# Optimization experiments

Measured on AMD Instinct MI355X. Metric: run time of the kernel, lower is better.

## Reference

```python
import math
import jax, jax.numpy as jnp
import numpy as np

E = 64   # embed_size (also per-head dim)
H = 8    # heads
B = 4
T = 2048


def setup_inputs() -> dict:
    key = jax.random.key(0)
    ks = jax.random.split(key, 8)
    s_in = 1.0 / math.sqrt(E)
    s_out = 1.0 / math.sqrt(H * E)
    return {
        "values": jax.random.normal(ks[0], (B, T, E), dtype=jnp.float32),
        "keys": jax.random.normal(ks[1], (B, T, E), dtype=jnp.float32),
        "queries": jax.random.normal(ks[2], (B, T, E), dtype=jnp.float32),
        # Linear(E, E*H, bias=False) weights, stored as [in, out] for x @ W
        "Wv": jax.random.uniform(ks[3], (E, E * H), jnp.float32, -s_in, s_in),
        "Wk": jax.random.uniform(ks[4], (E, E * H), jnp.float32, -s_in, s_in),
        "Wq": jax.random.uniform(ks[5], (E, E * H), jnp.float32, -s_in, s_in),
        # unifyheads: Linear(H*E, E)
        "Wu": jax.random.uniform(ks[6], (H * E, E), jnp.float32, -s_out, s_out),
        "bu": jax.random.uniform(ks[7], (E,), jnp.float32, -s_out, s_out),
    }


def reference(values, keys, queries, Wv, Wk, Wq, Wu, bu):
    b, t, e = keys.shape
    h = H
    v = (values @ Wv).reshape(b, t, h, e)   # bthe
    k = (keys @ Wk).reshape(b, t, h, e)
    q = (queries @ Wq).reshape(b, t, h, e)
    dot = jnp.einsum('bthe,bihe->bhti', q, k) / math.sqrt(e)  # [b,h,t,i]
    # NOTE: source applies softmax over dim=2 (the query axis t), faithfully kept
    attention = jax.nn.softmax(dot, axis=2)
    out = jnp.einsum('bhtd,bdhe->bthe', attention, v).reshape(b, t, h * e)
    return out @ Wu + bu
```

## Files before the change

### kernel.cpp

```cpp
#include <hip/hip_runtime.h>
#include <hip/hip_bf16.h>


typedef __attribute__((ext_vector_type(8))) __bf16 bf16x8;
typedef __attribute__((ext_vector_type(8))) unsigned short ushort8;
typedef __attribute__((ext_vector_type(4))) float f32x4;
typedef unsigned int uint32;

constexpr int B_ = 4;
constexpr int T_ = 2048;
constexpr int H_ = 8;
constexpr int E_ = 64;
constexpr int BH_ = B_ * H_;
constexpr float SCALE_ = 0.125f;

__device__ inline uint32 f2bf1(float f) {
  uint32 u = __builtin_bit_cast(uint32, f);
  return (u + 0x7fffu + ((u >> 16) & 1u)) >> 16;
}
__device__ inline uint32 pk2(float a, float b) {
  return f2bf1(a) | (f2bf1(b) << 16);
}
__device__ inline bf16x8 ld8(const unsigned short* p) {
  return __builtin_bit_cast(bf16x8, *(const ushort8*)p);
}
#define MFMA16(a, b, c) __builtin_amdgcn_mfma_f32_16x16x32_bf16(a, b, c, 0, 0, 0)

__global__ __launch_bounds__(512) void proj_bf16_kernel(
    const float* __restrict__ X, const float* __restrict__ W,
    unsigned short* __restrict__ Y, float scale) {
  constexpr int RT = 8;
  __shared__ float xs[RT][E_];
  const int row0 = blockIdx.x * RT;
  const int tid = threadIdx.x;
  {
    const int r = tid >> 6, c = tid & 63;
    xs[r][c] = X[(row0 + r) * E_ + c];
  }
  __syncthreads();
  const int j = tid;
  const int h = j >> 6, e = j & 63;
  float acc[RT];
#pragma unroll
  for (int r = 0; r < RT; ++r) acc[r] = 0.f;
  for (int c = 0; c < E_; ++c) {
    const float w = W[c * (H_ * E_) + j];
#pragma unroll
    for (int r = 0; r < RT; ++r) acc[r] += xs[r][c] * w;
  }
#pragma unroll
  for (int r = 0; r < RT; ++r) {
    const int row = row0 + r;
    const int b = row >> 11, t = row & (T_ - 1);
    Y[(((size_t)(b * H_ + h) * T_ + t) << 6) + e] =
        (unsigned short)f2bf1(acc[r] * scale);
  }
}

__global__ __launch_bounds__(512) void proj_f32_kernel(
    const float* __restrict__ X, const float* __restrict__ W,
    float* __restrict__ Y) {
  constexpr int RT = 8;
  __shared__ float xs[RT][E_];
  const int row0 = blockIdx.x * RT;
  const int tid = threadIdx.x;
  {
    const int r = tid >> 6, c = tid & 63;
    xs[r][c] = X[(row0 + r) * E_ + c];
  }
  __syncthreads();
  const int j = tid;
  const int h = j >> 6, e = j & 63;
  float acc[RT];
#pragma unroll
  for (int r = 0; r < RT; ++r) acc[r] = 0.f;
  for (int c = 0; c < E_; ++c) {
    const float w = W[c * (H_ * E_) + j];
#pragma unroll
    for (int r = 0; r < RT; ++r) acc[r] += xs[r][c] * w;
  }
#pragma unroll
  for (int r = 0; r < RT; ++r) {
    const int row = row0 + r;
    const int b = row >> 11, t = row & (T_ - 1);
    Y[(((size_t)(b * H_ + h) * T_ + t) << 6) + e] = acc[r];
  }
}

__global__ __launch_bounds__(256) void stats_kernel(
    const unsigned short* __restrict__ K16, const unsigned short* __restrict__ Q16,
    float* __restrict__ s_inv) {
  const int bh = blockIdx.y;
  const int tid = threadIdx.x;
  const int w = tid >> 6, lane = tid & 63;
  const int lm = lane & 15, lq = lane >> 4;
  const int d0 = blockIdx.x * 256 + w * 64;
  const unsigned short* Kp = K16 + (size_t)bh * T_ * E_;
  const unsigned short* Qp = Q16 + (size_t)bh * T_ * E_;

  bf16x8 kf[4][2];
#pragma unroll
  for (int dt = 0; dt < 4; ++dt) {
    kf[dt][0] = ld8(&Kp[(size_t)(d0 + dt * 16 + lm) * E_ + lq * 8]);
    kf[dt][1] = ld8(&Kp[(size_t)(d0 + dt * 16 + lm) * E_ + 32 + lq * 8]);
  }
  f32x4 sacc[4];
#pragma unroll
  for (int dt = 0; dt < 4; ++dt) sacc[dt] = (f32x4){0.f, 0.f, 0.f, 0.f};
  const f32x4 zero = {0.f, 0.f, 0.f, 0.f};

  for (int t0 = 0; t0 < T_; t0 += 16) {
    bf16x8 ql = ld8(&Qp[(size_t)(t0 + lm) * E_ + lq * 8]);
    bf16x8 qh = ld8(&Qp[(size_t)(t0 + lm) * E_ + 32 + lq * 8]);
#pragma unroll
    for (int dt = 0; dt < 4; ++dt) {
      f32x4 c = MFMA16(kf[dt][0], ql, zero);
      c = MFMA16(kf[dt][1], qh, c);
#pragma unroll
      for (int r = 0; r < 4; ++r) sacc[dt][r] += __expf(c[r]);
    }
  }
#pragma unroll
  for (int m = 1; m < 16; m <<= 1) {
#pragma unroll
    for (int dt = 0; dt < 4; ++dt)
#pragma unroll
      for (int r = 0; r < 4; ++r)
        sacc[dt][r] += __shfl_xor(sacc[dt][r], m);
  }
  if (lm == 0) {
#pragma unroll
    for (int dt = 0; dt < 4; ++dt)
#pragma unroll
      for (int r = 0; r < 4; ++r)
        s_inv[(size_t)bh * T_ + d0 + dt * 16 + lq * 4 + r] = 1.0f / sacc[dt][r];
  }
}

__global__ __launch_bounds__(256) void scale_kernel(
    const float* __restrict__ Vf, const float* __restrict__ s_inv,
    unsigned short* __restrict__ Vt16) {
  __shared__ float ts[64][68];
  const int bh = blockIdx.y;
  const int d0 = blockIdx.x * 64;
  const float* Vp = Vf + (size_t)bh * T_ * E_;
  const int tid = threadIdx.x;
  for (int idx = tid; idx < 64 * 16; idx += 256) {
    const int r = idx >> 4, c4 = idx & 15;
    const float4 v = *(const float4*)&Vp[(size_t)(d0 + r) * E_ + c4 * 4];
    const float is = s_inv[(size_t)bh * T_ + d0 + r];
    ts[r][c4 * 4 + 0] = v.x * is;
    ts[r][c4 * 4 + 1] = v.y * is;
    ts[r][c4 * 4 + 2] = v.z * is;
    ts[r][c4 * 4 + 3] = v.w * is;
  }
  __syncthreads();
  for (int idx = tid; idx < 64 * 16; idx += 256) {
    const int e = idx >> 4, d4 = idx & 15;
    uint2 o;
    o.x = pk2(ts[d4 * 4 + 0][e], ts[d4 * 4 + 1][e]);
    o.y = pk2(ts[d4 * 4 + 2][e], ts[d4 * 4 + 3][e]);
    *(uint2*)&Vt16[((size_t)bh * E_ + e) * T_ + d0 + d4 * 4] = o;
  }
}

__global__ __launch_bounds__(256) void apply_kernel(
    const unsigned short* __restrict__ K16, const unsigned short* __restrict__ Q16,
    const unsigned short* __restrict__ Vt16, float* __restrict__ o_ws) {
  __shared__ unsigned short es[4][32][40];
  const int bh = blockIdx.y;
  const int b = bh >> 3, h = bh & 7;
  const int tid = threadIdx.x;
  const int w = tid >> 6, lane = tid & 63;
  const int lm = lane & 15, lq = lane >> 4;
  const int t0 = blockIdx.x * 128 + w * 32;
  const unsigned short* Kp = K16 + (size_t)bh * T_ * E_;
  const unsigned short* Qp = Q16 + (size_t)bh * T_ * E_;
  const unsigned short* Vp = Vt16 + (size_t)bh * E_ * T_;

  bf16x8 qf[2][2];
#pragma unroll
  for (int tt = 0; tt < 2; ++tt) {
    qf[tt][0] = ld8(&Qp[(size_t)(t0 + tt * 16 + lm) * E_ + lq * 8]);
    qf[tt][1] = ld8(&Qp[(size_t)(t0 + tt * 16 + lm) * E_ + 32 + lq * 8]);
  }
  f32x4 acc[2][4];
#pragma unroll
  for (int tt = 0; tt < 2; ++tt)
#pragma unroll
    for (int ec = 0; ec < 4; ++ec) acc[tt][ec] = (f32x4){0.f, 0.f, 0.f, 0.f};
  const f32x4 zero = {0.f, 0.f, 0.f, 0.f};

  for (int d0 = 0; d0 < T_; d0 += 32) {
    const bf16x8 k0l = ld8(&Kp[(size_t)(d0 + lm) * E_ + lq * 8]);
    const bf16x8 k0h = ld8(&Kp[(size_t)(d0 + lm) * E_ + 32 + lq * 8]);
    const bf16x8 k1l = ld8(&Kp[(size_t)(d0 + 16 + lm) * E_ + lq * 8]);
    const bf16x8 k1h = ld8(&Kp[(size_t)(d0 + 16 + lm) * E_ + 32 + lq * 8]);
    bf16x8 vf[4];
#pragma unroll
    for (int ec = 0; ec < 4; ++ec)
      vf[ec] = ld8(&Vp[(size_t)(ec * 16 + lm) * T_ + d0 + lq * 8]);

#pragma unroll
    for (int tt = 0; tt < 2; ++tt) {
      f32x4 c0 = MFMA16(k0l, qf[tt][0], zero);
      c0 = MFMA16(k0h, qf[tt][1], c0);
      f32x4 c1 = MFMA16(k1l, qf[tt][0], zero);
      c1 = MFMA16(k1h, qf[tt][1], c1);
      float e0[4], e1[4];
#pragma unroll
      for (int r = 0; r < 4; ++r) { e0[r] = __expf(c0[r]); e1[r] = __expf(c1[r]); }
      *(uint2*)&es[w][tt * 16 + lm][lq * 4] =
          make_uint2(pk2(e0[0], e0[1]), pk2(e0[2], e0[3]));
      *(uint2*)&es[w][tt * 16 + lm][16 + lq * 4] =
          make_uint2(pk2(e1[0], e1[1]), pk2(e1[2], e1[3]));
    }
    asm volatile("s_waitcnt lgkmcnt(0)" ::: "memory");
#pragma unroll
    for (int tt = 0; tt < 2; ++tt) {
      const bf16x8 ae = ld8(&es[w][tt * 16 + lm][lq * 8]);
#pragma unroll
      for (int ec = 0; ec < 4; ++ec)
        acc[tt][ec] = MFMA16(ae, vf[ec], acc[tt][ec]);
    }
  }

#pragma unroll
  for (int tt = 0; tt < 2; ++tt) {
    const int t = t0 + tt * 16 + lq * 4;
#pragma unroll
    for (int ec = 0; ec < 4; ++ec) {
      const int e = ec * 16 + lm;
      float* op = &o_ws[((size_t)(b * T_ + t) * H_ + h) * E_ + e];
#pragma unroll
      for (int r = 0; r < 4; ++r) op[(size_t)r * H_ * E_] = acc[tt][ec][r];
    }
  }
}

__global__ __launch_bounds__(256) void unify_kernel(
    const float* __restrict__ o_ws, const float* __restrict__ Wu,
    const float* __restrict__ bu, float* __restrict__ out) {
  constexpr int RT = 16;
  __shared__ float xs[RT][H_ * E_];
  const int row0 = blockIdx.x * RT;
  const int tid = threadIdx.x;
  for (int idx = tid; idx < RT * 128; idx += 256) {
    const int r = idx >> 7, c4 = idx & 127;
    *(float4*)&xs[r][c4 * 4] = *(const float4*)&o_ws[(size_t)(row0 + r) * 512 + c4 * 4];
  }
  __syncthreads();
  const int j = tid & 63;
  const int rg = tid >> 6;
  float acc[4] = {0.f, 0.f, 0.f, 0.f};
  for (int c = 0; c < 512; ++c) {
    const float w = Wu[c * 64 + j];
#pragma unroll
    for (int r = 0; r < 4; ++r) acc[r] += xs[rg * 4 + r][c] * w;
  }
  const float bias = bu[j];
#pragma unroll
  for (int r = 0; r < 4; ++r)
    out[(size_t)(row0 + rg * 4 + r) * 64 + j] = acc[r] + bias;
}

extern "C" void kernel_launch(void* const* d_in, const int* in_sizes, int n_in,
                              void* d_out, int out_size, void* d_ws, size_t ws_size,
                              hipStream_t stream) {
  const float* values  = (const float*)d_in[0];
  const float* keys    = (const float*)d_in[1];
  const float* queries = (const float*)d_in[2];
  const float* Wv      = (const float*)d_in[3];
  const float* Wk      = (const float*)d_in[4];
  const float* Wq      = (const float*)d_in[5];
  const float* Wu      = (const float*)d_in[6];
  const float* bu      = (const float*)d_in[7];
  float* out = (float*)d_out;

  const size_t NQ = (size_t)BH_ * T_ * E_;
  unsigned short* q_bf = (unsigned short*)d_ws;
  unsigned short* k_bf = q_bf + NQ;
  unsigned short* vt_bf = k_bf + NQ;
  float* v_f  = (float*)(vt_bf + NQ);
  float* o_ws = v_f + NQ;
  float* s_inv = o_ws + NQ;

  proj_bf16_kernel<<<B_ * T_ / 8, 512, 0, stream>>>(queries, Wq, q_bf, SCALE_);
  proj_bf16_kernel<<<B_ * T_ / 8, 512, 0, stream>>>(keys, Wk, k_bf, 1.0f);
  proj_f32_kernel<<<B_ * T_ / 8, 512, 0, stream>>>(values, Wv, v_f);

  stats_kernel<<<dim3(T_ / 256, BH_), 256, 0, stream>>>(k_bf, q_bf, s_inv);
  scale_kernel<<<dim3(T_ / 64, BH_), 256, 0, stream>>>(v_f, s_inv, vt_bf);
  apply_kernel<<<dim3(T_ / 128, BH_), 256, 0, stream>>>(k_bf, q_bf, vt_bf, o_ws);
  unify_kernel<<<B_ * T_ / 16, 256, 0, stream>>>(o_ws, Wu, bu, out);
}
```

Measured before the change: 308.5 us.

## Fuse projections, split stats over query axis, prefetch K/V in apply, use exp2

```diff
diff --git a/kernel.cpp b/kernel.cpp
--- a/kernel.cpp
+++ b/kernel.cpp
@@ -1,5 +1,4 @@
 #include <hip/hip_runtime.h>
-#include <hip/hip_bf16.h>
 
 
 typedef __attribute__((ext_vector_type(8))) __bf16 bf16x8;
@@ -12,7 +11,8 @@
 constexpr int H_ = 8;
 constexpr int E_ = 64;
 constexpr int BH_ = B_ * H_;
-constexpr float SCALE_ = 0.125f;
+constexpr int SZ_ = 8;
+constexpr float QSCALE_ = 0.125f * 1.4426950408889634f;
 
 __device__ inline uint32 f2bf1(float f) {
   uint32 u = __builtin_bit_cast(uint32, f);
@@ -21,16 +21,28 @@
 __device__ inline uint32 pk2(float a, float b) {
   return f2bf1(a) | (f2bf1(b) << 16);
 }
+__device__ inline float bf2f(uint32 bits) {
+  return __builtin_bit_cast(float, bits << 16);
+}
 __device__ inline bf16x8 ld8(const unsigned short* p) {
   return __builtin_bit_cast(bf16x8, *(const ushort8*)p);
 }
 #define MFMA16(a, b, c) __builtin_amdgcn_mfma_f32_16x16x32_bf16(a, b, c, 0, 0, 0)
-
-__global__ __launch_bounds__(512) void proj_bf16_kernel(
-    const float* __restrict__ X, const float* __restrict__ W,
-    unsigned short* __restrict__ Y, float scale) {
+#define EXP2(x) __builtin_amdgcn_exp2f(x)
+
+__global__ __launch_bounds__(512) void proj_kernel(
+    const float* __restrict__ Xq, const float* __restrict__ Xk,
+    const float* __restrict__ Xv, const float* __restrict__ Wq,
+    const float* __restrict__ Wk, const float* __restrict__ Wv,
+    unsigned short* __restrict__ Yq, unsigned short* __restrict__ Yk,
+    unsigned short* __restrict__ Yv) {
   constexpr int RT = 8;
   __shared__ float xs[RT][E_];
+  const int z = blockIdx.y;
+  const float* X = (z == 0) ? Xq : (z == 1) ? Xk : Xv;
+  const float* W = (z == 0) ? Wq : (z == 1) ? Wk : Wv;
+  unsigned short* Y = (z == 0) ? Yq : (z == 1) ? Yk : Yv;
+  const float scale = (z == 0) ? QSCALE_ : 1.0f;
   const int row0 = blockIdx.x * RT;
   const int tid = threadIdx.x;
   {
@@ -57,44 +69,16 @@
   }
 }
 
-__global__ __launch_bounds__(512) void proj_f32_kernel(
-    const float* __restrict__ X, const float* __restrict__ W,
-    float* __restrict__ Y) {
-  constexpr int RT = 8;
-  __shared__ float xs[RT][E_];
-  const int row0 = blockIdx.x * RT;
-  const int tid = threadIdx.x;
-  {
-    const int r = tid >> 6, c = tid & 63;
-    xs[r][c] = X[(row0 + r) * E_ + c];
-  }
-  __syncthreads();
-  const int j = tid;
-  const int h = j >> 6, e = j & 63;
-  float acc[RT];
-#pragma unroll
-  for (int r = 0; r < RT; ++r) acc[r] = 0.f;
-  for (int c = 0; c < E_; ++c) {
-    const float w = W[c * (H_ * E_) + j];
-#pragma unroll
-    for (int r = 0; r < RT; ++r) acc[r] += xs[r][c] * w;
-  }
-#pragma unroll
-  for (int r = 0; r < RT; ++r) {
-    const int row = row0 + r;
-    const int b = row >> 11, t = row & (T_ - 1);
-    Y[(((size_t)(b * H_ + h) * T_ + t) << 6) + e] = acc[r];
-  }
-}
-
-__global__ __launch_bounds__(256) void stats_kernel(
+__global__ __launch_bounds__(256, 4) void stats_kernel(
     const unsigned short* __restrict__ K16, const unsigned short* __restrict__ Q16,
-    float* __restrict__ s_inv) {
+    float* __restrict__ s_part) {
   const int bh = blockIdx.y;
   const int tid = threadIdx.x;
   const int w = tid >> 6, lane = tid & 63;
   const int lm = lane & 15, lq = lane >> 4;
   const int d0 = blockIdx.x * 256 + w * 64;
+  const int tz0 = blockIdx.z * (T_ / SZ_);
+  const int tzend = tz0 + (T_ / SZ_);
   const unsigned short* Kp = K16 + (size_t)bh * T_ * E_;
   const unsigned short* Qp = Q16 + (size_t)bh * T_ * E_;
 
@@ -109,16 +93,20 @@
   for (int dt = 0; dt < 4; ++dt) sacc[dt] = (f32x4){0.f, 0.f, 0.f, 0.f};
   const f32x4 zero = {0.f, 0.f, 0.f, 0.f};
 
-  for (int t0 = 0; t0 < T_; t0 += 16) {
-    bf16x8 ql = ld8(&Qp[(size_t)(t0 + lm) * E_ + lq * 8]);
-    bf16x8 qh = ld8(&Qp[(size_t)(t0 + lm) * E_ + 32 + lq * 8]);
+  bf16x8 ql = ld8(&Qp[(size_t)(tz0 + lm) * E_ + lq * 8]);
+  bf16x8 qh = ld8(&Qp[(size_t)(tz0 + lm) * E_ + 32 + lq * 8]);
+  for (int t0 = tz0; t0 < tzend; t0 += 16) {
+    const int tn = (t0 + 16 < tzend) ? t0 + 16 : tz0;
+    bf16x8 nl = ld8(&Qp[(size_t)(tn + lm) * E_ + lq * 8]);
+    bf16x8 nh = ld8(&Qp[(size_t)(tn + lm) * E_ + 32 + lq * 8]);
 #pragma unroll
     for (int dt = 0; dt < 4; ++dt) {
       f32x4 c = MFMA16(kf[dt][0], ql, zero);
       c = MFMA16(kf[dt][1], qh, c);
 #pragma unroll
-      for (int r = 0; r < 4; ++r) sacc[dt][r] += __expf(c[r]);
+      for (int r = 0; r < 4; ++r) sacc[dt][r] += EXP2(c[r]);
     }
+    ql = nl; qh = nh;
   }
 #pragma unroll
   for (int m = 1; m < 16; m <<= 1) {
@@ -133,26 +121,34 @@
     for (int dt = 0; dt < 4; ++dt)
 #pragma unroll
       for (int r = 0; r < 4; ++r)
-        s_inv[(size_t)bh * T_ + d0 + dt * 16 + lq * 4 + r] = 1.0f / sacc[dt][r];
+        s_part[((size_t)blockIdx.z * BH_ + bh) * T_ + d0 + dt * 16 + lq * 4 + r] =
+            sacc[dt][r];
   }
 }
 
 __global__ __launch_bounds__(256) void scale_kernel(
-    const float* __restrict__ Vf, const float* __restrict__ s_inv,
+    const unsigned short* __restrict__ V16, const float* __restrict__ s_part,
     unsigned short* __restrict__ Vt16) {
   __shared__ float ts[64][68];
+  __shared__ float sinv_s[64];
   const int bh = blockIdx.y;
   const int d0 = blockIdx.x * 64;
-  const float* Vp = Vf + (size_t)bh * T_ * E_;
-  const int tid = threadIdx.x;
-  for (int idx = tid; idx < 64 * 16; idx += 256) {
-    const int r = idx >> 4, c4 = idx & 15;
-    const float4 v = *(const float4*)&Vp[(size_t)(d0 + r) * E_ + c4 * 4];
-    const float is = s_inv[(size_t)bh * T_ + d0 + r];
-    ts[r][c4 * 4 + 0] = v.x * is;
-    ts[r][c4 * 4 + 1] = v.y * is;
-    ts[r][c4 * 4 + 2] = v.z * is;
-    ts[r][c4 * 4 + 3] = v.w * is;
+  const unsigned short* Vp = V16 + (size_t)bh * T_ * E_;
+  const int tid = threadIdx.x;
+  if (tid < 64) {
+    float s = 0.f;
+#pragma unroll
+    for (int z = 0; z < SZ_; ++z)
+      s += s_part[((size_t)z * BH_ + bh) * T_ + d0 + tid];
+    sinv_s[tid] = 1.0f / s;
+  }
+  __syncthreads();
+  for (int idx = tid; idx < 64 * 8; idx += 256) {
+    const int r = idx >> 3, c8 = idx & 7;
+    const ushort8 v8 = *(const ushort8*)&Vp[(size_t)(d0 + r) * E_ + c8 * 8];
+    const float is = sinv_s[r];
+#pragma unroll
+    for (int k = 0; k < 8; ++k) ts[r][c8 * 8 + k] = bf2f(v8[k]) * is;
   }
   __syncthreads();
   for (int idx = tid; idx < 64 * 16; idx += 256) {
@@ -164,77 +160,72 @@
   }
 }
 
-__global__ __launch_bounds__(256) void apply_kernel(
+__global__ __launch_bounds__(256, 4) void apply_kernel(
     const unsigned short* __restrict__ K16, const unsigned short* __restrict__ Q16,
     const unsigned short* __restrict__ Vt16, float* __restrict__ o_ws) {
-  __shared__ unsigned short es[4][32][40];
+  __shared__ __attribute__((aligned(16))) unsigned short es[4][16][40];
   const int bh = blockIdx.y;
   const int b = bh >> 3, h = bh & 7;
   const int tid = threadIdx.x;
   const int w = tid >> 6, lane = tid & 63;
   const int lm = lane & 15, lq = lane >> 4;
-  const int t0 = blockIdx.x * 128 + w * 32;
+  const int t0 = blockIdx.x * 64 + w * 16;
   const unsigned short* Kp = K16 + (size_t)bh * T_ * E_;
   const unsigned short* Qp = Q16 + (size_t)bh * T_ * E_;
   const unsigned short* Vp = Vt16 + (size_t)bh * E_ * T_;
 
-  bf16x8 qf[2][2];
-#pragma unroll
-  for (int tt = 0; tt < 2; ++tt) {
-    qf[tt][0] = ld8(&Qp[(size_t)(t0 + tt * 16 + lm) * E_ + lq * 8]);
-    qf[tt][1] = ld8(&Qp[(size_t)(t0 + tt * 16 + lm) * E_ + 32 + lq * 8]);
-  }
-  f32x4 acc[2][4];
-#pragma unroll
-  for (int tt = 0; tt < 2; ++tt)
-#pragma unroll
-    for (int ec = 0; ec < 4; ++ec) acc[tt][ec] = (f32x4){0.f, 0.f, 0.f, 0.f};
+  const bf16x8 qf0 = ld8(&Qp[(size_t)(t0 + lm) * E_ + lq * 8]);
+  const bf16x8 qf1 = ld8(&Qp[(size_t)(t0 + lm) * E_ + 32 + lq * 8]);
+  f32x4 acc[4];
+#pragma unroll
+  for (int ec = 0; ec < 4; ++ec) acc[ec] = (f32x4){0.f, 0.f, 0.f, 0.f};
   const f32x4 zero = {0.f, 0.f, 0.f, 0.f};
 
+  bf16x8 ck0l = ld8(&Kp[(size_t)lm * E_ + lq * 8]);
+  bf16x8 ck0h = ld8(&Kp[(size_t)lm * E_ + 32 + lq * 8]);
+  bf16x8 ck1l = ld8(&Kp[(size_t)(16 + lm) * E_ + lq * 8]);
+  bf16x8 ck1h = ld8(&Kp[(size_t)(16 + lm) * E_ + 32 + lq * 8]);
+  bf16x8 cv[4];
+#pragma unroll
+  for (int ec = 0; ec < 4; ++ec)
+    cv[ec] = ld8(&Vp[(size_t)(ec * 16 + lm) * T_ + lq * 8]);
+
   for (int d0 = 0; d0 < T_; d0 += 32) {
-    const bf16x8 k0l = ld8(&Kp[(size_t)(d0 + lm) * E_ + lq * 8]);
-    const bf16x8 k0h = ld8(&Kp[(size_t)(d0 + lm) * E_ + 32 + lq * 8]);
-    const bf16x8 k1l = ld8(&Kp[(size_t)(d0 + 16 + lm) * E_ + lq * 8]);
-    const bf16x8 k1h = ld8(&Kp[(size_t)(d0 + 16 + lm) * E_ + 32 + lq * 8]);
-    bf16x8 vf[4];
+    const int dn = (d0 + 32) & (T_ - 1);
+    bf16x8 nk0l = ld8(&Kp[(size_t)(dn + lm) * E_ + lq * 8]);
+    bf16x8 nk0h = ld8(&Kp[(size_t)(dn + lm) * E_ + 32 + lq * 8]);
+    bf16x8 nk1l = ld8(&Kp[(size_t)(dn + 16 + lm) * E_ + lq * 8]);
+    bf16x8 nk1h = ld8(&Kp[(size_t)(dn + 16 + lm) * E_ + 32 + lq * 8]);
+    bf16x8 nv[4];
 #pragma unroll
     for (int ec = 0; ec < 4; ++ec)
-      vf[ec] = ld8(&Vp[(size_t)(ec * 16 + lm) * T_ + d0 + lq * 8]);
-
-#pragma unroll
-    for (int tt = 0; tt < 2; ++tt) {
-      f32x4 c0 = MFMA16(k0l, qf[tt][0], zero);
-      c0 = MFMA16(k0h, qf[tt][1], c0);
-      f32x4 c1 = MFMA16(k1l, qf[tt][0], zero);
-      c1 = MFMA16(k1h, qf[tt][1], c1);
-      float e0[4], e1[4];
-#pragma unroll
-      for (int r = 0; r < 4; ++r) { e0[r] = __expf(c0[r]); e1[r] = __expf(c1[r]); }
-      *(uint2*)&es[w][tt * 16 + lm][lq * 4] =
-          make_uint2(pk2(e0[0], e0[1]), pk2(e0[2], e0[3]));
-      *(uint2*)&es[w][tt * 16 + lm][16 + lq * 4] =
-          make_uint2(pk2(e1[0], e1[1]), pk2(e1[2], e1[3]));
-    }
+      nv[ec] = ld8(&Vp[(size_t)(ec * 16 + lm) * T_ + dn + lq * 8]);
+
+    f32x4 c0 = MFMA16(ck0l, qf0, zero);
+    c0 = MFMA16(ck0h, qf1, c0);
+    f32x4 c1 = MFMA16(ck1l, qf0, zero);
+    c1 = MFMA16(ck1h, qf1, c1);
+    float e0[4], e1[4];
+#pragma unroll
+    for (int r = 0; r < 4; ++r) { e0[r] = EXP2(c0[r]); e1[r] = EXP2(c1[r]); }
+    *(uint2*)&es[w][lm][lq * 4] = make_uint2(pk2(e0[0], e0[1]), pk2(e0[2], e0[3]));
+    *(uint2*)&es[w][lm][16 + lq * 4] = make_uint2(pk2(e1[0], e1[1]), pk2(e1[2], e1[3]));
     asm volatile("s_waitcnt lgkmcnt(0)" ::: "memory");
-#pragma unroll
-    for (int tt = 0; tt < 2; ++tt) {
-      const bf16x8 ae = ld8(&es[w][tt * 16 + lm][lq * 8]);
-#pragma unroll
-      for (int ec = 0; ec < 4; ++ec)
-        acc[tt][ec] = MFMA16(ae, vf[ec], acc[tt][ec]);
-    }
-  }
-
-#pragma unroll
-  for (int tt = 0; tt < 2; ++tt) {
-    const int t = t0 + tt * 16 + lq * 4;
-#pragma unroll
-    for (int ec = 0; ec < 4; ++ec) {
-      const int e = ec * 16 + lm;
-      float* op = &o_ws[((size_t)(b * T_ + t) * H_ + h) * E_ + e];
-#pragma unroll
-      for (int r = 0; r < 4; ++r) op[(size_t)r * H_ * E_] = acc[tt][ec][r];
-    }
+    const bf16x8 ae = ld8(&es[w][lm][lq * 8]);
+#pragma unroll
+    for (int ec = 0; ec < 4; ++ec) acc[ec] = MFMA16(ae, cv[ec], acc[ec]);
+
+    ck0l = nk0l; ck0h = nk0h; ck1l = nk1l; ck1h = nk1h;
+#pragma unroll
+    for (int ec = 0; ec < 4; ++ec) cv[ec] = nv[ec];
+  }
+
+#pragma unroll
+  for (int ec = 0; ec < 4; ++ec) {
+    const int e = ec * 16 + lm;
+    float* op = &o_ws[((size_t)(b * T_ + t0 + lq * 4) * H_ + h) * E_ + e];
+#pragma unroll
+    for (int r = 0; r < 4; ++r) op[(size_t)r * H_ * E_] = acc[ec][r];
   }
 }
 
@@ -278,19 +269,17 @@
   float* out = (float*)d_out;
 
   const size_t NQ = (size_t)BH_ * T_ * E_;
-  unsigned short* q_bf = (unsigned short*)d_ws;
-  unsigned short* k_bf = q_bf + NQ;
-  unsigned short* vt_bf = k_bf + NQ;
-  float* v_f  = (float*)(vt_bf + NQ);
-  float* o_ws = v_f + NQ;
-  float* s_inv = o_ws + NQ;
-
-  proj_bf16_kernel<<<B_ * T_ / 8, 512, 0, stream>>>(queries, Wq, q_bf, SCALE_);
-  proj_bf16_kernel<<<B_ * T_ / 8, 512, 0, stream>>>(keys, Wk, k_bf, 1.0f);
-  proj_f32_kernel<<<B_ * T_ / 8, 512, 0, stream>>>(values, Wv, v_f);
-
-  stats_kernel<<<dim3(T_ / 256, BH_), 256, 0, stream>>>(k_bf, q_bf, s_inv);
-  scale_kernel<<<dim3(T_ / 64, BH_), 256, 0, stream>>>(v_f, s_inv, vt_bf);
-  apply_kernel<<<dim3(T_ / 128, BH_), 256, 0, stream>>>(k_bf, q_bf, vt_bf, o_ws);
+  unsigned short* q_bf  = (unsigned short*)d_ws;
+  unsigned short* k_bf  = q_bf + NQ;
+  unsigned short* v_bf  = k_bf + NQ;
+  unsigned short* vt_bf = v_bf + NQ;
+  float* o_ws   = (float*)(vt_bf + NQ);
+  float* s_part = o_ws + NQ;
+
+  proj_kernel<<<dim3(B_ * T_ / 8, 3), 512, 0, stream>>>(
+      queries, keys, values, Wq, Wk, Wv, q_bf, k_bf, v_bf);
+  stats_kernel<<<dim3(T_ / 256, BH_, SZ_), 256, 0, stream>>>(k_bf, q_bf, s_part);
+  scale_kernel<<<dim3(T_ / 64, BH_), 256, 0, stream>>>(v_bf, s_part, vt_bf);
+  apply_kernel<<<dim3(T_ / 64, BH_), 256, 0, stream>>>(k_bf, q_bf, vt_bf, o_ws);
   unify_kernel<<<B_ * T_ / 16, 256, 0, stream>>>(o_ws, Wu, bu, out);
 }
```

Result: slower. 401.4 us (+30.1%).
